# Kernel optimization log

Measured on AMD Instinct MI355X. Metric: run time of the kernel, lower is better.

## Reference

```python
import jax, jax.numpy as jnp
import numpy as np

NUM_HEADS = 8

def setup_inputs() -> dict:
    key = jax.random.key(0)
    ks = jax.random.split(key, 5)
    B, N, C = 8, 16384, 256
    x = jax.random.normal(ks[0], (B, N, C), dtype=jnp.float32)
    Wq = jax.random.normal(ks[1], (C, C), dtype=jnp.float32) * 0.02
    Wkv = jax.random.normal(ks[2], (2 * C, C), dtype=jnp.float32) * 0.02
    Wproj = jax.random.normal(ks[3], (C, C), dtype=jnp.float32) * 0.02
    bproj = jnp.zeros((C,), dtype=jnp.float32)
    return {"x": x, "Wq": Wq, "Wkv": Wkv, "Wproj": Wproj, "bproj": bproj}


def reference(x, Wq, Wkv, Wproj, bproj):
    B, N, C = x.shape
    h = NUM_HEADS
    d = C // h
    # q, kv projections (torch Linear: x @ W.T)
    q = jnp.einsum('bnc,oc->bno', x, Wq).reshape(B, N, h, d).transpose(0, 2, 1, 3)   # [B,h,N,d]
    kv = jnp.einsum('bnc,oc->bno', x, Wkv).reshape(B, N, 2, h, d)
    k = kv[:, :, 0].transpose(0, 2, 1, 3)  # [B,h,N,d]
    v = kv[:, :, 1].transpose(0, 2, 1, 3)  # [B,h,N,d]
    # feature map: elu(x) + 1 (positive)
    q = jax.nn.elu(q) + 1.0
    k = jax.nn.elu(k) + 1.0
    # normalizer: q . sum_n k_n
    k_sum = k.sum(axis=2)                                    # [B,h,d]
    D_inv = 1.0 / jnp.maximum(jnp.einsum('bhnd,bhd->bhn', q, k_sum), 1e-6)  # [B,h,N]
    # linear-attention context: k^T @ v  ->  [B,h,d,d]
    context = jnp.einsum('bhnd,bhne->bhde', k, v)
    attn = jnp.einsum('bhnd,bhde->bhne', q, context) * D_inv[..., None]     # [B,h,N,d]
    out = attn.transpose(0, 2, 1, 3).reshape(B, N, C)
    out = jnp.einsum('bnc,oc->bno', out, Wproj) + bproj
    return out
```

## Files before the change

kernel.cpp:

```cpp
#include <hip/hip_runtime.h>
#include <hip/hip_bf16.h>
#include <cstdint>
#include <cstddef>

typedef __attribute__((ext_vector_type(8))) short short8;
typedef __attribute__((ext_vector_type(4))) float f32x4;

#define DEVI static __device__ __forceinline__

DEVI unsigned short f2bf(float f) {
  unsigned u = __float_as_uint(f);
  unsigned r = u + 0x7fffu + ((u >> 16) & 1u);
  return (unsigned short)(r >> 16);
}
DEVI float bf2f(unsigned short s) {
  return __uint_as_float(((unsigned)s) << 16);
}
DEVI unsigned pack2(float a, float b) {
  return (unsigned)f2bf(a) | ((unsigned)f2bf(b) << 16);
}

DEVI void gload16(const void* g, void* l) {
  __builtin_amdgcn_global_load_lds(
      (__attribute__((address_space(1))) void*)g,
      (__attribute__((address_space(3))) void*)l, 16, 0, 0);
}

__global__ __launch_bounds__(256) void prep_w(
    const float* __restrict__ Wq, const float* __restrict__ Wkv,
    const float* __restrict__ Wp, unsigned short* __restrict__ wcat,
    unsigned short* __restrict__ wpb) {
  int i = blockIdx.x * 256 + threadIdx.x;
  if (i < 196608) {
    float v = (i < 65536) ? Wq[i] : Wkv[i - 65536];
    wcat[i] = f2bf(v);
  } else {
    int j = i - 196608;
    wpb[j] = f2bf(Wp[j]);
  }
}

__global__ __launch_bounds__(512, 4) void qkv_ctx(
    const float* __restrict__ x, const unsigned short* __restrict__ wcat,
    unsigned short* __restrict__ Q, float* __restrict__ pctx,
    float* __restrict__ pksum) {
  const int t = threadIdx.x;
  const int lane = t & 63, w = t >> 6;
  const int wr = w >> 1, wc = w & 1;
  const int blk = blockIdx.x;
  const size_t row0 = (size_t)blk * 128;
  const int fr = lane & 15, fq = lane >> 4;

  __shared__ __align__(16) unsigned char smem[49152];
  unsigned char* const wb0 = smem;
  unsigned char* const wb1 = smem + 16384;
  unsigned char* const kT = smem + 32768;
  unsigned char* const vT = smem + 40960;

  const short ob = (short)0x3F80;
  const short8 ones = {ob, ob, ob, ob, ob, ob, ob, ob};

  short8 xfc[2][8];
#pragma unroll
  for (int i = 0; i < 2; ++i) {
    const float* xr = x + (row0 + wr * 32 + i * 16 + fr) * 256;
#pragma unroll
    for (int ks = 0; ks < 8; ++ks) {
      float4 a = *(const float4*)(xr + ks * 32 + fq * 8);
      float4 b2 = *(const float4*)(xr + ks * 32 + fq * 8 + 4);
      union { unsigned u[4]; short8 s; } cv;
      cv.u[0] = pack2(a.x, a.y);
      cv.u[1] = pack2(a.z, a.w);
      cv.u[2] = pack2(b2.x, b2.y);
      cv.u[3] = pack2(b2.z, b2.w);
      xfc[i][ks] = cv.s;
    }
  }

  const int segr = lane >> 5;
  const int segc = (lane & 31) * 16;
  auto stage_w = [&](unsigned char* buf, int s) {
    int wr0 = (s < 8) ? s * 32
                      : (((s & 1) == 0) ? 256 + ((s - 8) >> 1) * 32
                                        : 512 + ((s - 8) >> 1) * 32);
#pragma unroll
    for (int i = 0; i < 2; ++i) {
      int seg = w * 2 + i;
      int rloc = seg * 2 + segr;
      gload16((const char*)wcat + (size_t)(wr0 + rloc) * 512 +
                  (segc ^ ((rloc & 7) << 4)),
              buf + seg * 1024);
    }
  };

  auto ctx_head = [&](int h) {
    if (w < 4) {
      const int dp = w >> 1, ep = w & 1;
      f32x4 cacc = {0.f, 0.f, 0.f, 0.f};
      const int rka = dp * 16 + fr;
      const int rkb = ep * 16 + fr;
#pragma unroll
      for (int ks = 0; ks < 4; ++ks) {
        short8 ak = *(const short8*)(kT + rka * 256 +
                                     ((ks * 64 + fq * 16) ^ ((rka & 7) << 4)));
        short8 bv = *(const short8*)(vT + rkb * 256 +
                                     ((ks * 64 + fq * 16) ^ ((rkb & 7) << 4)));
        cacc = __builtin_amdgcn_mfma_f32_16x16x32_bf16(ak, bv, cacc, 0, 0, 0);
      }
      float* pc = pctx + ((size_t)(blk * 8 + h)) * 1024;
#pragma unroll
      for (int reg = 0; reg < 4; ++reg) {
        int d = dp * 16 + fq * 4 + reg;
        int e = ep * 16 + fr;
        pc[d * 32 + e] = cacc[reg];
      }
    }
  };

  auto ksum_head = [&](int h) {
    if ((w >> 1) == 2) {
      const int dp = w & 1;
      f32x4 sacc = {0.f, 0.f, 0.f, 0.f};
      const int rka = dp * 16 + fr;
#pragma unroll
      for (int ks = 0; ks < 4; ++ks) {
        short8 ak = *(const short8*)(kT + rka * 256 +
                                     ((ks * 64 + fq * 16) ^ ((rka & 7) << 4)));
        sacc = __builtin_amdgcn_mfma_f32_16x16x32_bf16(ak, ones, sacc, 0, 0, 0);
      }
      if (fr == 0) {
#pragma unroll
        for (int reg = 0; reg < 4; ++reg) {
          int d = dp * 16 + fq * 4 + reg;
          pksum[((size_t)(blk * 8 + h)) * 32 + d] = sacc[reg];
        }
      }
    }
  };

  stage_w(wb0, 0);
  __syncthreads();

  unsigned char* const bb = kT + w * 1536;

#pragma unroll
  for (int s = 0; s < 8; ++s) {
    stage_w((s & 1) ? wb0 : wb1, s + 1);
    const unsigned char* wbuf = (s & 1) ? wb1 : wb0;

    f32x4 acc[2] = {{0.f, 0.f, 0.f, 0.f}, {0.f, 0.f, 0.f, 0.f}};
    const int rb = wc * 16 + fr;
    const int swb = (rb & 7) << 4;
#pragma unroll
    for (int ks = 0; ks < 8; ++ks) {
      short8 wf = *(const short8*)(wbuf + rb * 512 + ((ks * 64 + fq * 16) ^ swb));
      acc[0] = __builtin_amdgcn_mfma_f32_16x16x32_bf16(wf, xfc[0][ks], acc[0], 0, 0, 0);
      acc[1] = __builtin_amdgcn_mfma_f32_16x16x32_bf16(wf, xfc[1][ks], acc[1], 0, 0, 0);
    }
#pragma unroll
    for (int i = 0; i < 2; ++i) {
      float v0 = acc[i][0], v1 = acc[i][1], v2 = acc[i][2], v3 = acc[i][3];
      v0 = (v0 > 0.f) ? (v0 + 1.f) : __expf(v0);
      v1 = (v1 > 0.f) ? (v1 + 1.f) : __expf(v1);
      v2 = (v2 > 0.f) ? (v2 + 1.f) : __expf(v2);
      v3 = (v3 > 0.f) ? (v3 + 1.f) : __expf(v3);
      uint2 pk;
      pk.x = pack2(v0, v1);
      pk.y = pack2(v2, v3);
      *(uint2*)(bb + (i * 16 + fr) * 48 + fq * 8) = pk;
    }
    {
      int rowq = lane >> 1, ch = lane & 1;
      uint4 u = *(const uint4*)(bb + rowq * 48 + ch * 16);
      *(uint4*)((char*)Q + (row0 + wr * 32 + rowq) * 512 + s * 64 + wc * 32 +
                ch * 16) = u;
    }
    __syncthreads();
  }

#pragma unroll
  for (int h = 0; h < 8; ++h) {
    const int sk = 8 + 2 * h;
    stage_w(wb1, sk + 1);
    f32x4 kacc[2] = {{0.f, 0.f, 0.f, 0.f}, {0.f, 0.f, 0.f, 0.f}};
    {
      const int rb = wc * 16 + fr;
      const int swb = (rb & 7) << 4;
#pragma unroll
      for (int ks = 0; ks < 8; ++ks) {
        short8 wf = *(const short8*)(wb0 + rb * 512 + ((ks * 64 + fq * 16) ^ swb));
        kacc[0] = __builtin_amdgcn_mfma_f32_16x16x32_bf16(xfc[0][ks], wf, kacc[0], 0, 0, 0);
        kacc[1] = __builtin_amdgcn_mfma_f32_16x16x32_bf16(xfc[1][ks], wf, kacc[1], 0, 0, 0);
      }
    }
    if (h > 0) {
      ctx_head(h - 1);
      ksum_head(h - 1);
    }
    __syncthreads();

#pragma unroll
    for (int i = 0; i < 2; ++i) {
      int d = wc * 16 + fr;
      float v0 = kacc[i][0], v1 = kacc[i][1], v2 = kacc[i][2], v3 = kacc[i][3];
      v0 = (v0 > 0.f) ? (v0 + 1.f) : __expf(v0);
      v1 = (v1 > 0.f) ? (v1 + 1.f) : __expf(v1);
      v2 = (v2 > 0.f) ? (v2 + 1.f) : __expf(v2);
      v3 = (v3 > 0.f) ? (v3 + 1.f) : __expf(v3);
      uint2 pk;
      pk.x = pack2(v0, v1);
      pk.y = pack2(v2, v3);
      int nb = wr * 64 + i * 32 + fq * 8;
      *(uint2*)(kT + d * 256 + (nb ^ ((d & 7) << 4))) = pk;
    }

    if (h < 7) stage_w(wb0, sk + 2);
    f32x4 vacc[2] = {{0.f, 0.f, 0.f, 0.f}, {0.f, 0.f, 0.f, 0.f}};
    {
      const int rb = wc * 16 + fr;
      const int swb = (rb & 7) << 4;
#pragma unroll
      for (int ks = 0; ks < 8; ++ks) {
        short8 wf = *(const short8*)(wb1 + rb * 512 + ((ks * 64 + fq * 16) ^ swb));
        vacc[0] = __builtin_amdgcn_mfma_f32_16x16x32_bf16(xfc[0][ks], wf, vacc[0], 0, 0, 0);
        vacc[1] = __builtin_amdgcn_mfma_f32_16x16x32_bf16(xfc[1][ks], wf, vacc[1], 0, 0, 0);
      }
    }
#pragma unroll
    for (int i = 0; i < 2; ++i) {
      int e = wc * 16 + fr;
      uint2 pk;
      pk.x = pack2(vacc[i][0], vacc[i][1]);
      pk.y = pack2(vacc[i][2], vacc[i][3]);
      int nb = wr * 64 + i * 32 + fq * 8;
      *(uint2*)(vT + e * 256 + (nb ^ ((e & 7) << 4))) = pk;
    }
    __syncthreads();
  }
  ctx_head(7);
  ksum_head(7);
}

__global__ __launch_bounds__(256) void ctx_final2(
    const float* __restrict__ pctx, const float* __restrict__ pksum,
    unsigned short* __restrict__ ctxT, float* __restrict__ ksum) {
  int bh = blockIdx.x;
  int b = bh >> 3, h = bh & 7;
  int t = threadIdx.x;
  int d = t >> 3, e4 = (t & 7) * 4;
  float s[4] = {0.f, 0.f, 0.f, 0.f};
  for (int pp = 0; pp < 128; ++pp) {
    const float* q = pctx + ((size_t)((b * 128 + pp) * 8 + h)) * 1024 + d * 32 + e4;
    s[0] += q[0]; s[1] += q[1]; s[2] += q[2]; s[3] += q[3];
  }
  unsigned short* cc = ctxT + (size_t)bh * 2048;
#pragma unroll
  for (int e2 = 0; e2 < 4; ++e2) {
    int e = e4 + e2;
    unsigned short hi = f2bf(s[e2]);
    float lo = s[e2] - bf2f(hi);
    cc[e * 32 + d] = hi;
    cc[1024 + e * 32 + d] = f2bf(lo);
  }
  __shared__ float ksp[8][32];
  int d2 = t & 31, ch = t >> 5;
  float ss = 0.f;
  for (int pp = ch; pp < 128; pp += 8)
    ss += pksum[((size_t)((b * 128 + pp) * 8 + h)) * 32 + d2];
  ksp[ch][d2] = ss;
  __syncthreads();
  if (t < 32) {
    float r = 0.f;
#pragma unroll
    for (int c = 0; c < 8; ++c) r += ksp[c][t];
    ksum[bh * 32 + t] = r;
  }
}

__global__ __launch_bounds__(512) void attn_proj(
    const unsigned short* __restrict__ Q,
    const unsigned short* __restrict__ ctxT,
    const float* __restrict__ ksum,
    const unsigned short* __restrict__ wpb,
    const float* __restrict__ bias,
    float* __restrict__ out) {
  const int t = threadIdx.x;
  const int lane = t & 63, w = t >> 6;
  const int panel = blockIdx.x;
  const int b = panel >> 8;
  const size_t row0 = (size_t)panel * 64;
  const int fr = lane & 15, fq = lane >> 4;

  __shared__ __align__(16) unsigned char qa[32768];
  __shared__ __align__(16) unsigned char wpS[2][16384];
  __shared__ float ksumL[256];
  __shared__ float Dinv_s[64][8];

#pragma unroll
  for (int s = 0; s < 4; ++s) {
    int seg = w * 4 + s;
    int row = seg * 2 + (lane >> 5);
    gload16((const char*)Q + (row0 + row) * 512 +
                (((lane & 31) * 16) ^ ((row & 7) << 4)),
            qa + seg * 1024);
  }
  if (w == 0) gload16((const char*)(ksum + b * 256) + lane * 16, (void*)ksumL);
  __syncthreads();

  {
    int r = t >> 3, h = t & 7;
    const unsigned char* qrow = qa + r * 512;
    int swzr = (r & 7) << 4;
    float s = 0.f;
#pragma unroll
    for (int dd = 0; dd < 16; ++dd) {
      unsigned u = *(const unsigned*)(qrow + ((h * 64 + dd * 4) ^ swzr));
      s += __uint_as_float(u << 16) * ksumL[h * 32 + dd * 2] +
           __uint_as_float(u & 0xffff0000u) * ksumL[h * 32 + dd * 2 + 1];
    }
    Dinv_s[r][h] = 1.f / fmaxf(s, 1e-6f);
  }

  const int rg = w >> 2, hg = w & 3;
  f32x4 sacc[2][2][2];
#pragma unroll
  for (int h2 = 0; h2 < 2; ++h2)
#pragma unroll
    for (int i = 0; i < 2; ++i)
#pragma unroll
      for (int j = 0; j < 2; ++j)
#pragma unroll
        for (int c = 0; c < 4; ++c) sacc[h2][i][j][c] = 0.f;

#pragma unroll
  for (int h2 = 0; h2 < 2; ++h2) {
    int h = hg * 2 + h2;
    const char* cbh = (const char*)ctxT + ((size_t)(b * 8 + h)) * 4096;
    short8 bhi[2], blo[2];
#pragma unroll
    for (int j = 0; j < 2; ++j) {
      int e = j * 16 + fr;
      bhi[j] = *(const short8*)(cbh + e * 64 + fq * 16);
      blo[j] = *(const short8*)(cbh + 2048 + e * 64 + fq * 16);
    }
#pragma unroll
    for (int i = 0; i < 2; ++i) {
      int ra = rg * 32 + i * 16 + fr;
      short8 af = *(const short8*)(qa + ra * 512 +
                                   ((h * 64 + fq * 16) ^ ((ra & 7) << 4)));
#pragma unroll
      for (int j = 0; j < 2; ++j) {
        sacc[h2][i][j] = __builtin_amdgcn_mfma_f32_16x16x32_bf16(
            af, bhi[j], sacc[h2][i][j], 0, 0, 0);
        sacc[h2][i][j] = __builtin_amdgcn_mfma_f32_16x16x32_bf16(
            af, blo[j], sacc[h2][i][j], 0, 0, 0);
      }
    }
  }
  __syncthreads();

#pragma unroll
  for (int h2 = 0; h2 < 2; ++h2) {
    int h = hg * 2 + h2;
#pragma unroll
    for (int i = 0; i < 2; ++i)
#pragma unroll
      for (int j = 0; j < 2; ++j)
#pragma unroll
        for (int reg = 0; reg < 4; ++reg) {
          int r = rg * 32 + i * 16 + fq * 4 + reg;
          int e = j * 16 + fr;
          float v = sacc[h2][i][j][reg] * Dinv_s[r][h];
          *(unsigned short*)(qa + r * 512 +
                             ((h * 64 + e * 2) ^ ((r & 7) << 4))) = f2bf(v);
        }
  }

  auto stage_wp = [&](int q, unsigned char* buf) {
#pragma unroll
    for (int i = 0; i < 2; ++i) {
      int seg = w * 2 + i;
      int rloc = seg * 2 + (lane >> 5);
      gload16((const char*)wpb + (size_t)(q * 32 + rloc) * 512 +
                  (((lane & 31) * 16) ^ ((rloc & 7) << 4)),
              buf + seg * 1024);
    }
  };
  stage_wp(0, wpS[0]);
  __syncthreads();

  const int rw = w >> 1, cw = w & 1;
  const int ra2 = rw * 16 + fr;
  const int sra2 = (ra2 & 7) << 4;
  for (int q = 0; q < 8; ++q) {
    if (q < 7) stage_wp(q + 1, wpS[(q + 1) & 1]);
    const unsigned char* wbuf = wpS[q & 1];
    f32x4 oacc = {0.f, 0.f, 0.f, 0.f};
#pragma unroll
    for (int ks = 0; ks < 8; ++ks) {
      short8 af = *(const short8*)(qa + ra2 * 512 + ((ks * 64 + fq * 16) ^ sra2));
      int rb = cw * 16 + fr;
      short8 wf = *(const short8*)(wbuf + rb * 512 +
                                   ((ks * 64 + fq * 16) ^ ((rb & 7) << 4)));
      oacc = __builtin_amdgcn_mfma_f32_16x16x32_bf16(af, wf, oacc, 0, 0, 0);
    }
    float bj = bias[q * 32 + cw * 16 + fr];
    float* orow = out + row0 * 256 + (size_t)(rw * 16 + fq * 4) * 256 +
                  q * 32 + cw * 16 + fr;
#pragma unroll
    for (int reg = 0; reg < 4; ++reg) orow[reg * 256] = oacc[reg] + bj;
    __syncthreads();
  }
}

extern "C" void kernel_launch(void* const* d_in, const int* in_sizes, int n_in,
                              void* d_out, int out_size, void* d_ws, size_t ws_size,
                              hipStream_t stream) {
  const float* x = (const float*)d_in[0];
  const float* Wq = (const float*)d_in[1];
  const float* Wkv = (const float*)d_in[2];
  const float* Wproj = (const float*)d_in[3];
  const float* bproj = (const float*)d_in[4];
  float* out = (float*)d_out;

  char* ws = (char*)d_ws;
  unsigned short* Q = (unsigned short*)(ws);
  unsigned short* wcat = (unsigned short*)(ws + 67108864);
  unsigned short* wpb = (unsigned short*)(ws + 67502080);
  float* pctx = (float*)(ws + 67633152);
  float* pksum = (float*)(ws + 101187584);
  unsigned short* ctxT = (unsigned short*)(ws + 102236160);
  float* ksum = (float*)(ws + 102498304);

  prep_w<<<1024, 256, 0, stream>>>(Wq, Wkv, Wproj, wcat, wpb);
  qkv_ctx<<<1024, 512, 0, stream>>>(x, wcat, Q, pctx, pksum);
  ctx_final2<<<64, 256, 0, stream>>>(pctx, pksum, ctxT, ksum);
  attn_proj<<<2048, 512, 0, stream>>>(Q, ctxT, ksum, wpb, bproj, out);
}
```

Measured before the change: 174.0 us.

## Triple-buffer weight staging with explicit vmcnt-based barriers in qkv_ctx

```diff
diff --git a/kernel.cpp b/kernel.cpp
--- a/kernel.cpp
+++ b/kernel.cpp
@@ -25,6 +25,11 @@
       (__attribute__((address_space(1))) void*)g,
       (__attribute__((address_space(3))) void*)l, 16, 0, 0);
 }
+
+#define SYNCA2 do { asm volatile("s_waitcnt vmcnt(2) lgkmcnt(0)" ::: "memory"); __builtin_amdgcn_s_barrier(); } while (0)
+#define SYNCA3 do { asm volatile("s_waitcnt vmcnt(3) lgkmcnt(0)" ::: "memory"); __builtin_amdgcn_s_barrier(); } while (0)
+#define SYNCA0 do { asm volatile("s_waitcnt vmcnt(0) lgkmcnt(0)" ::: "memory"); __builtin_amdgcn_s_barrier(); } while (0)
+#define SYNCB  do { asm volatile("s_waitcnt lgkmcnt(0)" ::: "memory"); __builtin_amdgcn_s_barrier(); } while (0)
 
 __global__ __launch_bounds__(256) void prep_w(
     const float* __restrict__ Wq, const float* __restrict__ Wkv,
@@ -51,11 +56,9 @@
   const size_t row0 = (size_t)blk * 128;
   const int fr = lane & 15, fq = lane >> 4;
 
-  __shared__ __align__(16) unsigned char smem[49152];
-  unsigned char* const wb0 = smem;
-  unsigned char* const wb1 = smem + 16384;
-  unsigned char* const kT = smem + 32768;
-  unsigned char* const vT = smem + 40960;
+  __shared__ __align__(16) unsigned char smem[65536];
+  unsigned char* const kT = smem + 49152;
+  unsigned char* const vT = smem + 57344;
 
   const short ob = (short)0x3F80;
   const short8 ones = {ob, ob, ob, ob, ob, ob, ob, ob};
@@ -138,15 +141,16 @@
     }
   };
 
-  stage_w(wb0, 0);
-  __syncthreads();
+  stage_w(smem, 0);
+  stage_w(smem + 16384, 1);
 
   unsigned char* const bb = kT + w * 1536;
 
 #pragma unroll
   for (int s = 0; s < 8; ++s) {
-    stage_w((s & 1) ? wb0 : wb1, s + 1);
-    const unsigned char* wbuf = (s & 1) ? wb1 : wb0;
+    if (s == 0) { SYNCA2; } else { SYNCA3; }
+    stage_w(smem + ((s + 2) % 3) * 16384, s + 2);
+    const unsigned char* wbuf = smem + (s % 3) * 16384;
 
     f32x4 acc[2] = {{0.f, 0.f, 0.f, 0.f}, {0.f, 0.f, 0.f, 0.f}};
     const int rb = wc * 16 + fr;
@@ -175,20 +179,21 @@
       *(uint4*)((char*)Q + (row0 + wr * 32 + rowq) * 512 + s * 64 + wc * 32 +
                 ch * 16) = u;
     }
-    __syncthreads();
   }
 
 #pragma unroll
   for (int h = 0; h < 8; ++h) {
-    const int sk = 8 + 2 * h;
-    stage_w(wb1, sk + 1);
+    const int sk = 8 + 2 * h, sv = sk + 1;
+    if (h == 0) { SYNCA3; } else { SYNCA2; }
+    if (sk + 2 < 24) stage_w(smem + ((sk + 2) % 3) * 16384, sk + 2);
     f32x4 kacc[2] = {{0.f, 0.f, 0.f, 0.f}, {0.f, 0.f, 0.f, 0.f}};
     {
+      const unsigned char* wbuf = smem + (sk % 3) * 16384;
       const int rb = wc * 16 + fr;
       const int swb = (rb & 7) << 4;
 #pragma unroll
       for (int ks = 0; ks < 8; ++ks) {
-        short8 wf = *(const short8*)(wb0 + rb * 512 + ((ks * 64 + fq * 16) ^ swb));
+        short8 wf = *(const short8*)(wbuf + rb * 512 + ((ks * 64 + fq * 16) ^ swb));
         kacc[0] = __builtin_amdgcn_mfma_f32_16x16x32_bf16(xfc[0][ks], wf, kacc[0], 0, 0, 0);
         kacc[1] = __builtin_amdgcn_mfma_f32_16x16x32_bf16(xfc[1][ks], wf, kacc[1], 0, 0, 0);
       }
@@ -197,7 +202,7 @@
       ctx_head(h - 1);
       ksum_head(h - 1);
     }
-    __syncthreads();
+    SYNCB;
 
 #pragma unroll
     for (int i = 0; i < 2; ++i) {
@@ -214,14 +219,20 @@
       *(uint2*)(kT + d * 256 + (nb ^ ((d & 7) << 4))) = pk;
     }
 
-    if (h < 7) stage_w(wb0, sk + 2);
+    if (sv + 2 < 24) {
+      SYNCA2;
+      stage_w(smem + ((sv + 2) % 3) * 16384, sv + 2);
+    } else {
+      SYNCA0;
+    }
     f32x4 vacc[2] = {{0.f, 0.f, 0.f, 0.f}, {0.f, 0.f, 0.f, 0.f}};
     {
+      const unsigned char* wbuf = smem + (sv % 3) * 16384;
       const int rb = wc * 16 + fr;
       const int swb = (rb & 7) << 4;
 #pragma unroll
       for (int ks = 0; ks < 8; ++ks) {
-        short8 wf = *(const short8*)(wb1 + rb * 512 + ((ks * 64 + fq * 16) ^ swb));
+        short8 wf = *(const short8*)(wbuf + rb * 512 + ((ks * 64 + fq * 16) ^ swb));
         vacc[0] = __builtin_amdgcn_mfma_f32_16x16x32_bf16(xfc[0][ks], wf, vacc[0], 0, 0, 0);
         vacc[1] = __builtin_amdgcn_mfma_f32_16x16x32_bf16(xfc[1][ks], wf, vacc[1], 0, 0, 0);
       }
@@ -235,8 +246,8 @@
       int nb = wr * 64 + i * 32 + fq * 8;
       *(uint2*)(vT + e * 256 + (nb ^ ((e & 7) << 4))) = pk;
     }
-    __syncthreads();
-  }
+  }
+  SYNCB;
   ctx_head(7);
   ksum_head(7);
 }
```

After: 261.8 us. +50.5%, slower.
